# Kernel tuning notes

Hardware: AMD Instinct MI355X
Metric: run time of the kernel (lower is better)

## Reference

```python
import jax, jax.numpy as jnp
import numpy as np

N, K, A = 4096, 64, 8      # nodes, level-2 paths per node, attrs per l2-neighbor
D = 128                    # embed_dim
NU, NR, NA = 100000, 32, 5000  # user vocab, rating vocab, attribute vocab


def setup_inputs() -> dict:
    key = jax.random.key(0)
    ks = jax.random.split(key, 12)
    s = 0.02
    return dict(
        nodes=jax.random.randint(ks[0], (N,), 0, NU),
        paths_rel=jax.random.randint(ks[1], (N, K, 2), 0, NR),
        paths_nbr=jax.random.randint(ks[2], (N, K), 0, NU),
        attrs=jax.random.randint(ks[3], (N, K, A), 0, NA),
        u2e=jax.random.normal(ks[4], (NU, D), dtype=jnp.float32) * s,
        r2e=jax.random.normal(ks[5], (NR, D), dtype=jnp.float32) * s,
        ua2e=jax.random.normal(ks[6], (NA, D), dtype=jnp.float32) * s,
        W1=jax.random.normal(ks[7], (4 * D, 2 * D), dtype=jnp.float32) * s,
        b1=jnp.zeros((2 * D,), jnp.float32),
        W2=jax.random.normal(ks[8], (2 * D, D), dtype=jnp.float32) * s,
        b2=jnp.zeros((D,), jnp.float32),
        A1=jax.random.normal(ks[9], (2 * D, D), dtype=jnp.float32) * s,
        ab1=jnp.zeros((D,), jnp.float32),
        A2=jax.random.normal(ks[10], (D, D), dtype=jnp.float32) * s,
        ab2=jnp.zeros((D,), jnp.float32),
        A3=jax.random.normal(ks[11], (D, 1), dtype=jnp.float32) * s,
        ab3=jnp.zeros((1,), jnp.float32),
    )


def reference(nodes, paths_rel, paths_nbr, attrs, u2e, r2e, ua2e,
              W1, b1, W2, b2, A1, ab1, A2, ab2, A3, ab3):
    # per-path embedding gathers
    r1 = r2e[paths_rel[..., 0]]           # [N,K,D]
    r2 = r2e[paths_rel[..., 1]]           # [N,K,D]
    ne = u2e[paths_nbr]                   # [N,K,D]
    ae = ua2e[attrs].sum(axis=2)          # [N,K,A,D] -> [N,K,D] (uvAttrEmbedding sum)
    # concat + 2-layer MLP (w_r1, w_r2)
    x = jnp.concatenate([r1, r2, ne, ae], axis=-1)   # [N,K,4D]
    h = jax.nn.relu(x @ W1 + b1)                     # [N,K,2D]
    h = jax.nn.relu(h @ W2 + b2)                     # [N,K,D]
    # attention vs self embedding
    self_e = u2e[nodes]                              # [N,D]
    c = jnp.concatenate(
        [h, jnp.broadcast_to(self_e[:, None, :], h.shape)], axis=-1)  # [N,K,2D]
    a = jax.nn.relu(c @ A1 + ab1)
    a = jax.nn.relu(a @ A2 + ab2)
    logits = (a @ A3 + ab3)[..., 0]                  # [N,K]
    w = jax.nn.softmax(logits, axis=1)
    # attention-weighted reduce over paths
    return jnp.einsum('nk,nkd->nd', w, h)            # [N,D]
```

## Files before the change

### kernel.cpp

```cpp
#include <hip/hip_runtime.h>
#include <hip/hip_bf16.h>

#define NN 4096
#define KK 64
#define AA 8
#define DD 128

#define XH_STRIDE 264
#define A_STRIDE  136
#define H2_STRIDE 136
#define XREG_SZ   16896

typedef __bf16 bf16x8 __attribute__((ext_vector_type(8)));
typedef __bf16 bf16x2 __attribute__((ext_vector_type(2)));
typedef float  f32x4  __attribute__((ext_vector_type(4)));

__device__ __forceinline__ short f2bf(float f) {
    unsigned u = __builtin_bit_cast(unsigned, f);
    u += 0x7FFFu + ((u >> 16) & 1u);
    return (short)(u >> 16);
}
__device__ __forceinline__ float bf2f(short s) {
    unsigned u = ((unsigned)(unsigned short)s) << 16;
    return __builtin_bit_cast(float, u);
}
__device__ __forceinline__ unsigned f2bf2(float a, float b) {
#if __has_builtin(__builtin_amdgcn_cvt_pk_bf16_f32)
    bf16x2 r = __builtin_amdgcn_cvt_pk_bf16_f32(a, b);
    return __builtin_bit_cast(unsigned, r);
#else
    return ((unsigned)(unsigned short)f2bf(a)) | (((unsigned)(unsigned short)f2bf(b)) << 16);
#endif
}
__device__ __forceinline__ void store_bf8(short* dst, float4 a, float4 b) {
    uint4 v;
    v.x = f2bf2(a.x, a.y); v.y = f2bf2(a.z, a.w);
    v.z = f2bf2(b.x, b.y); v.w = f2bf2(b.z, b.w);
    *(uint4*)dst = v;
}

__global__ void prep_all(const float* __restrict__ W1, const float* __restrict__ W2,
                         const float* __restrict__ A1, const float* __restrict__ A2,
                         const int* __restrict__ nodes, const float* __restrict__ u2e,
                         const float* __restrict__ ab1,
                         short* __restrict__ W1p, short* __restrict__ W2p,
                         short* __restrict__ A1p, short* __restrict__ A2p,
                         float* __restrict__ s1g)
{
    if (blockIdx.x < 96) {
        const int t    = blockIdx.x * 256 + threadIdx.x;
        const int idx8 = t * 8;
        const float* src; short* dst; int Ncols, ksl, idx;
        if (idx8 < 131072)      { src = W1; dst = W1p; Ncols = 256; ksl = 4; idx = idx8; }
        else if (idx8 < 163840) { src = W2; dst = W2p; Ncols = 128; ksl = 3; idx = idx8 - 131072; }
        else if (idx8 < 180224) { src = A1; dst = A1p; Ncols = 128; ksl = 2; idx = idx8 - 163840; }
        else                    { src = A2; dst = A2p; Ncols = 128; ksl = 2; idx = idx8 - 180224; }
        const int lane  = (idx >> 3) & 63;
        const int fi    = idx >> 9;
        const int kstep = fi & ((1 << ksl) - 1);
        const int ntile = fi >> ksl;
        const int k0 = kstep * 32 + (lane >> 4) * 8;
        const int nn = ntile * 16 + (lane & 15);
        short v[8];
#pragma unroll
        for (int j = 0; j < 8; ++j)
            v[j] = f2bf(src[(size_t)(k0 + j) * Ncols + nn]);
        *(uint4*)&dst[idx] = *(const uint4*)v;
    } else {
        __shared__ float rows[8][DD];
        const int b = blockIdx.x - 96;
        {
            const int r  = threadIdx.x >> 5;
            const int c4 = (threadIdx.x & 31) * 4;
            const int node = nodes[b * 8 + r];
            *(float4*)&rows[r][c4] = *(const float4*)&u2e[(size_t)node * DD + c4];
        }
        __syncthreads();
        const int h = threadIdx.x >> 7;
        const int c = threadIdx.x & 127;
        const float ab = ab1[c];
        float acc[4] = {ab, ab, ab, ab};
#pragma unroll 4
        for (int i = 0; i < DD; ++i) {
            const float av = A1[(size_t)(DD + i) * DD + c];
#pragma unroll
            for (int j = 0; j < 4; ++j)
                acc[j] = fmaf(rows[h * 4 + j][i], av, acc[j]);
        }
#pragma unroll
        for (int j = 0; j < 4; ++j)
            s1g[(size_t)(b * 8 + h * 4 + j) * DD + c] = acc[j];
    }
}

__launch_bounds__(512, 4)
__global__ void l2agg_mfma(
    const int* __restrict__ paths_rel,
    const int* __restrict__ paths_nbr,
    const int* __restrict__ attrs,
    const float* __restrict__ u2e,
    const float* __restrict__ r2e,
    const float* __restrict__ ua2e,
    const float* __restrict__ b1,
    const float* __restrict__ b2,
    const float* __restrict__ ab2,
    const float* __restrict__ A3,
    const float* __restrict__ ab3,
    const short* __restrict__ W1p,
    const short* __restrict__ W2p,
    const short* __restrict__ A1p,
    const short* __restrict__ A2p,
    const float* __restrict__ s1g,
    float* __restrict__ out)
{
    __shared__ short xa[XREG_SZ];
    __shared__ short xb[XREG_SZ];
    __shared__ int   idx_u[576];
    __shared__ float wts8[512];
    float* partials = (float*)idx_u;

    const int n    = blockIdx.x;
    const int tid  = threadIdx.x;
    const int lane = tid & 63;
    const int wv   = tid >> 6;
    const int mr   = lane & 15;
    const int q    = lane >> 4;

    {
        const int* ab = attrs + (size_t)n * KK * AA;
        __builtin_amdgcn_global_load_lds(
            (const __attribute__((address_space(1))) void*)(ab + wv * 64 + lane),
            (__attribute__((address_space(3))) void*)(idx_u + wv * 64), 4, 0, 0);
        if (wv == 0) {
            const int* nb = paths_nbr + (size_t)n * KK;
            __builtin_amdgcn_global_load_lds(
                (const __attribute__((address_space(1))) void*)(nb + lane),
                (__attribute__((address_space(3))) void*)(idx_u + 512), 4, 0, 0);
        }
    }

#pragma unroll
    for (int pass = 0; pass < 2; ++pass) {
        const int p  = pass * 32 + (tid >> 4);
        const int t  = tid & 15;
        const int o  = t * 8;
        const int pk = n * KK + p;
        const int i0 = paths_rel[pk * 2 + 0];
        const int i1 = paths_rel[pk * 2 + 1];
        float4 r1a = *(const float4*)&r2e[(size_t)i0 * DD + o];
        float4 r1b = *(const float4*)&r2e[(size_t)i0 * DD + o + 4];
        float4 r2a = *(const float4*)&r2e[(size_t)i1 * DD + o];
        float4 r2b = *(const float4*)&r2e[(size_t)i1 * DD + o + 4];
        store_bf8(&xa[p * XH_STRIDE + o], r1a, r1b);
        store_bf8(&xa[p * XH_STRIDE + 128 + o], r2a, r2b);
    }
    __syncthreads();

    const short* W1b = W1p + wv * 2 * 16 * 512 + lane * 8;
    f32x4 acc1[4][2] = {};
    bf16x8 bfc[2], bfn[2];
#pragma unroll
    for (int nt = 0; nt < 2; ++nt) bfc[nt] = *(const bf16x8*)&W1b[nt * 8192];
#pragma unroll
    for (int ks = 0; ks < 8; ++ks) {
#pragma unroll
        for (int nt = 0; nt < 2; ++nt)
            bfn[nt] = *(const bf16x8*)&W1b[nt * 8192 + (ks + 1) * 512];
        bf16x8 af[4];
#pragma unroll
        for (int mt = 0; mt < 4; ++mt)
            af[mt] = *(const bf16x8*)&xa[(mt * 16 + mr) * XH_STRIDE + ks * 32 + q * 8];
#pragma unroll
        for (int nt = 0; nt < 2; ++nt)
#pragma unroll
            for (int mt = 0; mt < 4; ++mt)
                acc1[mt][nt] = __builtin_amdgcn_mfma_f32_16x16x32_bf16(af[mt], bfc[nt], acc1[mt][nt], 0, 0, 0);
#pragma unroll
        for (int nt = 0; nt < 2; ++nt) bfc[nt] = bfn[nt];
    }

    __builtin_amdgcn_sched_barrier(0);

#pragma unroll
    for (int pass = 0; pass < 2; ++pass) {
        const int p  = pass * 32 + (tid >> 4);
        const int t  = tid & 15;
        const int o  = t * 8;
        const int nb = idx_u[512 + p];
        float4 nea = *(const float4*)&u2e[(size_t)nb * DD + o];
        float4 neb = *(const float4*)&u2e[(size_t)nb * DD + o + 4];
        float4 aea = make_float4(0.f, 0.f, 0.f, 0.f);
        float4 aeb = make_float4(0.f, 0.f, 0.f, 0.f);
#pragma unroll
        for (int a = 0; a < AA; ++a) {
            const int ai = idx_u[p * AA + a];
            float4 va = *(const float4*)&ua2e[(size_t)ai * DD + o];
            float4 vb = *(const float4*)&ua2e[(size_t)ai * DD + o + 4];
            aea.x += va.x; aea.y += va.y; aea.z += va.z; aea.w += va.w;
            aeb.x += vb.x; aeb.y += vb.y; aeb.z += vb.z; aeb.w += vb.w;
        }
        store_bf8(&xb[p * XH_STRIDE + o], nea, neb);
        store_bf8(&xb[p * XH_STRIDE + 128 + o], aea, aeb);
    }
    __builtin_amdgcn_sched_barrier(0);
    __syncthreads();

#pragma unroll
    for (int ks = 8; ks < 16; ++ks) {
        if (ks < 15) {
#pragma unroll
            for (int nt = 0; nt < 2; ++nt)
                bfn[nt] = *(const bf16x8*)&W1b[nt * 8192 + (ks + 1) * 512];
        }
        bf16x8 af[4];
#pragma unroll
        for (int mt = 0; mt < 4; ++mt)
            af[mt] = *(const bf16x8*)&xb[(mt * 16 + mr) * XH_STRIDE + (ks - 8) * 32 + q * 8];
#pragma unroll
        for (int nt = 0; nt < 2; ++nt)
#pragma unroll
            for (int mt = 0; mt < 4; ++mt)
                acc1[mt][nt] = __builtin_amdgcn_mfma_f32_16x16x32_bf16(af[mt], bfc[nt], acc1[mt][nt], 0, 0, 0);
        if (ks < 15) {
#pragma unroll
            for (int nt = 0; nt < 2; ++nt) bfc[nt] = bfn[nt];
        }
    }

    const short* W2b = W2p + wv * 8 * 512 + lane * 8;
    bf16x8 g2c = *(const bf16x8*)&W2b[0], g2n;

#pragma unroll
    for (int nt = 0; nt < 2; ++nt) {
        const int col = (wv * 2 + nt) * 16 + mr;
        const float bb = b1[col];
#pragma unroll
        for (int mt = 0; mt < 4; ++mt)
#pragma unroll
            for (int r = 0; r < 4; r += 2) {
                unsigned pk2 = f2bf2(fmaxf(acc1[mt][nt][r] + bb, 0.f),
                                     fmaxf(acc1[mt][nt][r + 1] + bb, 0.f));
                xa[(mt * 16 + q * 4 + r)     * XH_STRIDE + col] = (short)pk2;
                xa[(mt * 16 + q * 4 + r + 1) * XH_STRIDE + col] = (short)(pk2 >> 16);
            }
    }
    __syncthreads();

    f32x4 acc2[4] = {};
#pragma unroll
    for (int ks = 0; ks < 8; ++ks) {
        if (ks < 7) g2n = *(const bf16x8*)&W2b[(ks + 1) * 512];
        bf16x8 af[4];
#pragma unroll
        for (int mt = 0; mt < 4; ++mt)
            af[mt] = *(const bf16x8*)&xa[(mt * 16 + mr) * XH_STRIDE + ks * 32 + q * 8];
#pragma unroll
        for (int mt = 0; mt < 4; ++mt)
            acc2[mt] = __builtin_amdgcn_mfma_f32_16x16x32_bf16(af[mt], g2c, acc2[mt], 0, 0, 0);
        if (ks < 7) g2c = g2n;
    }

    const short* A1b = A1p + wv * 4 * 512 + lane * 8;
    bf16x8 g3f[4];
#pragma unroll
    for (int ks = 0; ks < 4; ++ks) g3f[ks] = *(const bf16x8*)&A1b[ks * 512];
    const float s1v = s1g[(size_t)n * DD + wv * 16 + mr];

    {
        const int col = wv * 16 + mr;
        const float bb = b2[col];
#pragma unroll
        for (int mt = 0; mt < 4; ++mt)
#pragma unroll
            for (int r = 0; r < 4; r += 2) {
                unsigned pk2 = f2bf2(fmaxf(acc2[mt][r] + bb, 0.f),
                                     fmaxf(acc2[mt][r + 1] + bb, 0.f));
                xb[(mt * 16 + q * 4 + r)     * H2_STRIDE + col] = (short)pk2;
                xb[(mt * 16 + q * 4 + r + 1) * H2_STRIDE + col] = (short)(pk2 >> 16);
            }
    }
    __syncthreads();

    {
        f32x4 acc3[4];
#pragma unroll
        for (int mt = 0; mt < 4; ++mt) {
            acc3[mt][0] = s1v; acc3[mt][1] = s1v; acc3[mt][2] = s1v; acc3[mt][3] = s1v;
        }
#pragma unroll
        for (int ks = 0; ks < 4; ++ks) {
            bf16x8 af[4];
#pragma unroll
            for (int mt = 0; mt < 4; ++mt)
                af[mt] = *(const bf16x8*)&xb[(mt * 16 + mr) * H2_STRIDE + ks * 32 + q * 8];
#pragma unroll
            for (int mt = 0; mt < 4; ++mt)
                acc3[mt] = __builtin_amdgcn_mfma_f32_16x16x32_bf16(af[mt], g3f[ks], acc3[mt], 0, 0, 0);
        }
        const short* A2b = A2p + wv * 4 * 512 + lane * 8;
        bf16x8 g4f[4];
#pragma unroll
        for (int ks = 0; ks < 4; ++ks) g4f[ks] = *(const bf16x8*)&A2b[ks * 512];

        {
            const int col = wv * 16 + mr;
#pragma unroll
            for (int mt = 0; mt < 4; ++mt)
#pragma unroll
                for (int r = 0; r < 4; r += 2) {
                    unsigned pk2 = f2bf2(fmaxf(acc3[mt][r], 0.f),
                                         fmaxf(acc3[mt][r + 1], 0.f));
                    xa[(mt * 16 + q * 4 + r)     * A_STRIDE + col] = (short)pk2;
                    xa[(mt * 16 + q * 4 + r + 1) * A_STRIDE + col] = (short)(pk2 >> 16);
                }
        }
        __syncthreads();

        f32x4 acc4[4];
        {
            const float bv = ab2[wv * 16 + mr];
#pragma unroll
            for (int mt = 0; mt < 4; ++mt) {
                acc4[mt][0] = bv; acc4[mt][1] = bv; acc4[mt][2] = bv; acc4[mt][3] = bv;
            }
        }
#pragma unroll
        for (int ks = 0; ks < 4; ++ks) {
            bf16x8 af[4];
#pragma unroll
            for (int mt = 0; mt < 4; ++mt)
                af[mt] = *(const bf16x8*)&xa[(mt * 16 + mr) * A_STRIDE + ks * 32 + q * 8];
#pragma unroll
            for (int mt = 0; mt < 4; ++mt)
                acc4[mt] = __builtin_amdgcn_mfma_f32_16x16x32_bf16(af[mt], g4f[ks], acc4[mt], 0, 0, 0);
        }
        const float av = A3[wv * 16 + mr];
        float pl[4][4];
#pragma unroll
        for (int mt = 0; mt < 4; ++mt)
#pragma unroll
            for (int r = 0; r < 4; ++r)
                pl[mt][r] = fmaxf(acc4[mt][r], 0.f) * av;
#pragma unroll
        for (int off = 1; off < 16; off <<= 1)
#pragma unroll
            for (int mt = 0; mt < 4; ++mt)
#pragma unroll
                for (int r = 0; r < 4; ++r)
                    pl[mt][r] += __shfl_xor(pl[mt][r], off, 64);
        if (mr == 0) {
#pragma unroll
            for (int mt = 0; mt < 4; ++mt)
#pragma unroll
                for (int r = 0; r < 4; ++r)
                    partials[wv * KK + mt * 16 + q * 4 + r] = pl[mt][r];
        }
    }
    __syncthreads();

    {
        float l = ab3[0];
#pragma unroll
        for (int w = 0; w < 8; ++w) l += partials[w * KK + lane];
        float m = l;
#pragma unroll
        for (int off = 32; off > 0; off >>= 1) m = fmaxf(m, __shfl_xor(m, off, 64));
        float e = expf(l - m);
        float s = e;
#pragma unroll
        for (int off = 32; off > 0; off >>= 1) s += __shfl_xor(s, off, 64);
        wts8[wv * 64 + lane] = e / s;
        const int col = wv * 16 + mr;
        const float* wl = &wts8[wv * 64 + q * 16];
        const short* hp = &xb[(q * 16) * H2_STRIDE + col];
        float acc = 0.f;
#pragma unroll
        for (int j = 0; j < 16; ++j)
            acc = fmaf(wl[j], bf2f(hp[j * H2_STRIDE]), acc);
        acc += __shfl_xor(acc, 16, 64);
        acc += __shfl_xor(acc, 32, 64);
        if (q == 0) out[(size_t)n * DD + col] = acc;
    }
}

extern "C" void kernel_launch(void* const* d_in, const int* in_sizes, int n_in,
                              void* d_out, int out_size, void* d_ws, size_t ws_size,
                              hipStream_t stream)
{
    const int*   nodes     = (const int*)d_in[0];
    const int*   paths_rel = (const int*)d_in[1];
    const int*   paths_nbr = (const int*)d_in[2];
    const int*   attrs     = (const int*)d_in[3];
    const float* u2e  = (const float*)d_in[4];
    const float* r2e  = (const float*)d_in[5];
    const float* ua2e = (const float*)d_in[6];
    const float* W1   = (const float*)d_in[7];
    const float* b1   = (const float*)d_in[8];
    const float* W2   = (const float*)d_in[9];
    const float* b2   = (const float*)d_in[10];
    const float* A1   = (const float*)d_in[11];
    const float* ab1  = (const float*)d_in[12];
    const float* A2   = (const float*)d_in[13];
    const float* ab2  = (const float*)d_in[14];
    const float* A3   = (const float*)d_in[15];
    const float* ab3  = (const float*)d_in[16];
    float* out = (float*)d_out;

    short* wsp = (short*)d_ws;
    short* W1p = wsp;
    short* W2p = wsp + 131072;
    short* A1p = wsp + 163840;
    short* A2p = wsp + 180224;
    float* s1g = (float*)((char*)d_ws + 393216);

    hipLaunchKernelGGL(prep_all, dim3(96 + 512), dim3(256), 0, stream,
                       W1, W2, A1, A2, nodes, u2e, ab1,
                       W1p, W2p, A1p, A2p, s1g);
    hipLaunchKernelGGL(l2agg_mfma, dim3(NN), dim3(512), 0, stream,
                       paths_rel, paths_nbr, attrs, u2e, r2e, ua2e,
                       b1, b2, ab2, A3, ab3,
                       W1p, W2p, A1p, A2p, s1g, out);
}
```

Before: 292.3 us.

## Pre-convert embedding tables to bf16 and gather half-width rows

```diff
diff --git a/kernel.cpp b/kernel.cpp
--- a/kernel.cpp
+++ b/kernel.cpp
@@ -93,6 +93,24 @@
     }
 }
 
+__global__ void conv_bf16(const float* __restrict__ u2e, const float* __restrict__ r2e,
+                          const float* __restrict__ ua2e,
+                          short* __restrict__ u2b, short* __restrict__ r2b,
+                          short* __restrict__ uab)
+{
+    const int t  = blockIdx.x * 256 + threadIdx.x;
+    const int e8 = t * 8;
+    const float* src; short* dst; int off;
+    if (e8 < 12800000)      { src = u2e;  dst = u2b; off = e8; }
+    else if (e8 < 12804096) { src = r2e;  dst = r2b; off = e8 - 12800000; }
+    else if (e8 < 13444096) { src = ua2e; dst = uab; off = e8 - 12804096; }
+    else return;
+    float4 a = *(const float4*)&src[off];
+    float4 b = *(const float4*)&src[off + 4];
+    store_bf8(&dst[off], a, b);
+}
+
+template<bool BFT>
 __launch_bounds__(512, 4)
 __global__ void l2agg_mfma(
     const int* __restrict__ paths_rel,
@@ -101,6 +119,9 @@
     const float* __restrict__ u2e,
     const float* __restrict__ r2e,
     const float* __restrict__ ua2e,
+    const short* __restrict__ u2b,
+    const short* __restrict__ r2b,
+    const short* __restrict__ uab,
     const float* __restrict__ b1,
     const float* __restrict__ b2,
     const float* __restrict__ ab2,
@@ -147,12 +168,19 @@
         const int pk = n * KK + p;
         const int i0 = paths_rel[pk * 2 + 0];
         const int i1 = paths_rel[pk * 2 + 1];
-        float4 r1a = *(const float4*)&r2e[(size_t)i0 * DD + o];
-        float4 r1b = *(const float4*)&r2e[(size_t)i0 * DD + o + 4];
-        float4 r2a = *(const float4*)&r2e[(size_t)i1 * DD + o];
-        float4 r2b = *(const float4*)&r2e[(size_t)i1 * DD + o + 4];
-        store_bf8(&xa[p * XH_STRIDE + o], r1a, r1b);
-        store_bf8(&xa[p * XH_STRIDE + 128 + o], r2a, r2b);
+        if constexpr (BFT) {
+            uint4 v1 = *(const uint4*)&r2b[(size_t)i0 * DD + o];
+            uint4 v2 = *(const uint4*)&r2b[(size_t)i1 * DD + o];
+            *(uint4*)&xa[p * XH_STRIDE + o]       = v1;
+            *(uint4*)&xa[p * XH_STRIDE + 128 + o] = v2;
+        } else {
+            float4 r1a = *(const float4*)&r2e[(size_t)i0 * DD + o];
+            float4 r1b = *(const float4*)&r2e[(size_t)i0 * DD + o + 4];
+            float4 r2a = *(const float4*)&r2e[(size_t)i1 * DD + o];
+            float4 r2b_ = *(const float4*)&r2e[(size_t)i1 * DD + o + 4];
+            store_bf8(&xa[p * XH_STRIDE + o], r1a, r1b);
+            store_bf8(&xa[p * XH_STRIDE + 128 + o], r2a, r2b_);
+        }
     }
     __syncthreads();
 
@@ -187,20 +215,43 @@
         const int t  = tid & 15;
         const int o  = t * 8;
         const int nb = idx_u[512 + p];
-        float4 nea = *(const float4*)&u2e[(size_t)nb * DD + o];
-        float4 neb = *(const float4*)&u2e[(size_t)nb * DD + o + 4];
-        float4 aea = make_float4(0.f, 0.f, 0.f, 0.f);
-        float4 aeb = make_float4(0.f, 0.f, 0.f, 0.f);
-#pragma unroll
-        for (int a = 0; a < AA; ++a) {
-            const int ai = idx_u[p * AA + a];
-            float4 va = *(const float4*)&ua2e[(size_t)ai * DD + o];
-            float4 vb = *(const float4*)&ua2e[(size_t)ai * DD + o + 4];
-            aea.x += va.x; aea.y += va.y; aea.z += va.z; aea.w += va.w;
-            aeb.x += vb.x; aeb.y += vb.y; aeb.z += vb.z; aeb.w += vb.w;
-        }
-        store_bf8(&xb[p * XH_STRIDE + o], nea, neb);
-        store_bf8(&xb[p * XH_STRIDE + 128 + o], aea, aeb);
+        if constexpr (BFT) {
+            uint4 nev = *(const uint4*)&u2b[(size_t)nb * DD + o];
+            float aes[8] = {0.f, 0.f, 0.f, 0.f, 0.f, 0.f, 0.f, 0.f};
+#pragma unroll
+            for (int a = 0; a < AA; ++a) {
+                const int ai = idx_u[p * AA + a];
+                uint4 w = *(const uint4*)&uab[(size_t)ai * DD + o];
+                aes[0] += __builtin_bit_cast(float, w.x << 16);
+                aes[1] += __builtin_bit_cast(float, w.x & 0xFFFF0000u);
+                aes[2] += __builtin_bit_cast(float, w.y << 16);
+                aes[3] += __builtin_bit_cast(float, w.y & 0xFFFF0000u);
+                aes[4] += __builtin_bit_cast(float, w.z << 16);
+                aes[5] += __builtin_bit_cast(float, w.z & 0xFFFF0000u);
+                aes[6] += __builtin_bit_cast(float, w.w << 16);
+                aes[7] += __builtin_bit_cast(float, w.w & 0xFFFF0000u);
+            }
+            *(uint4*)&xb[p * XH_STRIDE + o] = nev;
+            uint4 pv;
+            pv.x = f2bf2(aes[0], aes[1]); pv.y = f2bf2(aes[2], aes[3]);
+            pv.z = f2bf2(aes[4], aes[5]); pv.w = f2bf2(aes[6], aes[7]);
+            *(uint4*)&xb[p * XH_STRIDE + 128 + o] = pv;
+        } else {
+            float4 nea = *(const float4*)&u2e[(size_t)nb * DD + o];
+            float4 neb = *(const float4*)&u2e[(size_t)nb * DD + o + 4];
+            float4 aea = make_float4(0.f, 0.f, 0.f, 0.f);
+            float4 aeb = make_float4(0.f, 0.f, 0.f, 0.f);
+#pragma unroll
+            for (int a = 0; a < AA; ++a) {
+                const int ai = idx_u[p * AA + a];
+                float4 va = *(const float4*)&ua2e[(size_t)ai * DD + o];
+                float4 vb = *(const float4*)&ua2e[(size_t)ai * DD + o + 4];
+                aea.x += va.x; aea.y += va.y; aea.z += va.z; aea.w += va.w;
+                aeb.x += vb.x; aeb.y += vb.y; aeb.z += vb.z; aeb.w += vb.w;
+            }
+            store_bf8(&xb[p * XH_STRIDE + o], nea, neb);
+            store_bf8(&xb[p * XH_STRIDE + 128 + o], aea, aeb);
+        }
     }
     __builtin_amdgcn_sched_barrier(0);
     __syncthreads();
@@ -412,12 +463,23 @@
     short* A1p = wsp + 163840;
     short* A2p = wsp + 180224;
     float* s1g = (float*)((char*)d_ws + 393216);
-
-    hipLaunchKernelGGL(prep_all, dim3(96 + 512), dim3(256), 0, stream,
-                       W1, W2, A1, A2, nodes, u2e, ab1,
-                       W1p, W2p, A1p, A2p, s1g);
-    hipLaunchKernelGGL(l2agg_mfma, dim3(NN), dim3(512), 0, stream,
-                       paths_rel, paths_nbr, attrs, u2e, r2e, ua2e,
-                       b1, b2, ab2, A3, ab3,
-                       W1p, W2p, A1p, A2p, s1g, out);
-}
+    short* u2b = (short*)((char*)d_ws + 2490368);
+    short* r2b = (short*)((char*)d_ws + 28090368);
+    short* uab = (short*)((char*)d_ws + 28098560);
+
+    const size_t WS_NEED = 29378560;
+    const bool bft = (ws_size >= WS_NEED);
+
+    prep_all<<<dim3(96 + 512), dim3(256), 0, stream>>>(
+        W1, W2, A1, A2, nodes, u2e, ab1, W1p, W2p, A1p, A2p, s1g);
+    if (bft) {
+        conv_bf16<<<dim3(6565), dim3(256), 0, stream>>>(u2e, r2e, ua2e, u2b, r2b, uab);
+        l2agg_mfma<true><<<dim3(NN), dim3(512), 0, stream>>>(
+            paths_rel, paths_nbr, attrs, u2e, r2e, ua2e, u2b, r2b, uab,
+            b1, b2, ab2, A3, ab3, W1p, W2p, A1p, A2p, s1g, out);
+    } else {
+        l2agg_mfma<false><<<dim3(NN), dim3(512), 0, stream>>>(
+            paths_rel, paths_nbr, attrs, u2e, r2e, ua2e, u2b, r2b, uab,
+            b1, b2, ab2, A3, ab3, W1p, W2p, A1p, A2p, s1g, out);
+    }
+}
```

After: 274.1 us. 6.2% less time.
